# Optimization experiments

Hardware: AMD Instinct MI355X
Metric: run time of the kernel (lower is better)

## Reference

```python
import jax, jax.numpy as jnp
import numpy as np

B, S, D, H = 512, 128, 2, 512


def _lstm_cell(x, h, c, Wih, Whh, bih, bhh):
    # PyTorch gate order: i, f, g, o
    z = x @ Wih.T + h @ Whh.T + bih + bhh
    i, f, g, o = jnp.split(z, 4, axis=-1)
    c = jax.nn.sigmoid(f) * c + jax.nn.sigmoid(i) * jnp.tanh(g)
    h = jax.nn.sigmoid(o) * jnp.tanh(c)
    return h, c


def setup_inputs() -> dict:
    key = jax.random.key(0)
    ks = jax.random.split(key, 18)
    sc = 1.0 / np.sqrt(H)
    u = lambda k, shape: jax.random.uniform(k, shape, jnp.float32, -sc, sc)
    return {
        "inp": jax.random.normal(ks[0], (B, S, D), jnp.float32),
        "enc_Wih": u(ks[1], (4 * H, D)),
        "enc_Whh": u(ks[2], (4 * H, H)),
        "enc_bih": u(ks[3], (4 * H,)),
        "enc_bhh": u(ks[4], (4 * H,)),
        "dec_Wih": u(ks[5], (4 * H, D)),
        "dec_Whh": u(ks[6], (4 * H, H)),
        "dec_bih": u(ks[7], (4 * H,)),
        "dec_bhh": u(ks[8], (4 * H,)),
        "W1": u(ks[9], (H, H)),
        "b1": u(ks[10], (H,)),
        "W2": u(ks[11], (H, H)),
        "b2": u(ks[12], (H,)),
        "v_w": u(ks[13], (H,)),
        "v_b": u(ks[14], (1,)),
        "comb_W": u(ks[15], (H, 2 * H)),
        "comb_b": u(ks[16], (H,)),
    }


def reference(inp, enc_Wih, enc_Whh, enc_bih, enc_bhh,
              dec_Wih, dec_Whh, dec_bih, dec_bhh,
              W1, b1, W2, b2, v_w, v_b, comb_W, comb_b):
    Bb, Ss, _ = inp.shape
    xs = jnp.transpose(inp, (1, 0, 2))  # [S,B,D]

    # --- encoder LSTM (1 layer) ---
    def enc_step(carry, x):
        h, c = carry
        h, c = _lstm_cell(x, h, c, enc_Wih, enc_Whh, enc_bih, enc_bhh)
        return (h, c), h

    h0 = jnp.zeros((Bb, H), inp.dtype)
    (h_enc, c_enc), enc_out = jax.lax.scan(enc_step, (h0, h0), xs)  # enc_out: [S,B,H]

    W1e = enc_out @ W1.T + b1            # [S,B,H]
    enc_bt = jnp.transpose(enc_out, (1, 0, 2))  # [B,S,H]

    # --- pointer decoder ---
    def dec_step(carry, _):
        h, c, cur = carry
        h, c = _lstm_cell(cur, h, c, dec_Wih, dec_Whh, dec_bih, dec_bhh)
        q = h @ W2.T + b2                               # [B,H]
        u = jnp.tanh(W1e + q[None]) @ v_w + v_b[0]      # [S,B]
        a = jax.nn.softmax(u.T, axis=1)                 # [B,S]
        chosen = jnp.argmax(a, axis=1)                  # [B]
        cur = jnp.take_along_axis(inp, chosen[:, None, None], axis=1)[:, 0, :]  # [B,D]
        ctx = jnp.einsum('bs,bsh->bh', a, enc_bt)       # [B,H]
        h = jnp.concatenate([ctx, h], axis=1) @ comb_W.T + comb_b
        return (h, c, cur), a

    cur0 = jnp.full((Bb, D), -1.0, inp.dtype)
    _, outs = jax.lax.scan(dec_step, (h_enc, c_enc, cur0), None, length=Ss)
    return jnp.transpose(outs, (1, 0, 2))  # [B,S,S]
```

## Files before the change

### kernel.cpp

```cpp
#include <hip/hip_runtime.h>

#define PB 512
#define PS 128
#define PD 2
#define PH 512
#define P4H 2048

typedef unsigned int u32;
typedef unsigned short u16;
typedef __attribute__((ext_vector_type(8))) short short8;
typedef __attribute__((ext_vector_type(4))) float f32x4;

__device__ __forceinline__ float fast_sigmoid(float x) {
    return __fdividef(1.0f, 1.0f + __expf(-x));
}
__device__ __forceinline__ float fast_tanh(float x) {
    float ax = fabsf(x);
    float e = __expf(-2.0f * ax);
    float r = __fdividef(1.0f - e, 1.0f + e);
    return x < 0.0f ? -r : r;
}

__device__ __forceinline__ float bf_dec_u(u16 v) { return __uint_as_float((u32)v << 16); }
__device__ __forceinline__ u16 bf_trunc(float v) { return (u16)(__float_as_uint(v) >> 16); }
__device__ __forceinline__ u16 bf_rne(float v) {
    u32 u = __float_as_uint(v);
    return (u16)((u + 0x7FFFu + ((u >> 16) & 1u)) >> 16);
}
__device__ __forceinline__ void bf_split(float v, u16& hi, u16& lo) {
    hi = bf_trunc(v);
    lo = bf_rne(v - bf_dec_u(hi));
}

struct CF32 {
    using T = float;
    static __device__ __forceinline__ float dec(T v) { return v; }
    static __device__ __forceinline__ T enc(float v) { return v; }
    static __device__ __forceinline__ void dec4(const T* p, float* o) {
        float4 v = *(const float4*)p; o[0]=v.x; o[1]=v.y; o[2]=v.z; o[3]=v.w;
    }
};
struct CBF16 {
    using T = u16;
    static __device__ __forceinline__ float dec(T v) { return __uint_as_float((u32)v << 16); }
    static __device__ __forceinline__ T enc(float v) { return bf_rne(v); }
    static __device__ __forceinline__ void dec4(const T* p, float* o) {
        uint2 v = *(const uint2*)p;
        o[0] = __uint_as_float(v.x << 16);
        o[1] = __uint_as_float(v.x & 0xFFFF0000u);
        o[2] = __uint_as_float(v.y << 16);
        o[3] = __uint_as_float(v.y & 0xFFFF0000u);
    }
};

__global__ __launch_bounds__(256) void prep_whh(
    const float* __restrict__ Whh, u16* __restrict__ hi, u16* __restrict__ lo)
{
    int np = blockIdx.x;
    int j = np >> 2, g = np & 3;
    const float* src = Whh + (size_t)(g * PH + j) * PH;
    for (int k = threadIdx.x; k < PH; k += 256) {
        u16 h_, l_;
        bf_split(src[k], h_, l_);
        hi[(size_t)np * PH + k] = h_;
        lo[(size_t)np * PH + k] = l_;
    }
}
__global__ __launch_bounds__(256) void prep_split(
    const float* __restrict__ W, u16* __restrict__ hi, u16* __restrict__ lo, int K)
{
    int n = blockIdx.x;
    const float* src = W + (size_t)n * K;
    for (int k = threadIdx.x; k < K; k += 256) {
        u16 h_, l_;
        bf_split(src[k], h_, l_);
        hi[(size_t)n * K + k] = h_;
        lo[(size_t)n * K + k] = l_;
    }
}
__global__ __launch_bounds__(256) void prep_small(
    const float* __restrict__ Wih, const float* __restrict__ bih,
    const float* __restrict__ bhh, float* __restrict__ wihp, float* __restrict__ bs)
{
    int np = blockIdx.x * 256 + threadIdx.x;
    if (np >= P4H) return;
    int j = np >> 2, g = np & 3;
    int n = g * PH + j;
    wihp[np * 2]     = Wih[(size_t)n * PD];
    wihp[np * 2 + 1] = Wih[(size_t)n * PD + 1];
    bs[np] = bih[n] + bhh[n];
}

template<int EXTRA_MODE>
__global__ __launch_bounds__(256) void lstm_fused(
    const u16* __restrict__ Whh_hi, const u16* __restrict__ Whh_lo,
    const float* __restrict__ wih_perm, const float* __restrict__ bsum,
    const float* __restrict__ x, int x_stride,
    const float* __restrict__ h_in,
    float* __restrict__ cT,
    float* __restrict__ h_out,
    void* __restrict__ extra)
{
    __shared__ u16 As_hi[64][72];
    __shared__ u16 As_lo[64][72];
    __shared__ u16 Bs_hi[64][72];
    __shared__ u16 Bs_lo[64][72];

    const int tid = threadIdx.x;
    const int bb = blockIdx.x * 64;
    const int bn = blockIdx.y * 64;
    const int w = tid >> 6;
    const int wm = w >> 1, wn = w & 1;
    const int lane = tid & 63;
    const int l15 = lane & 15, lq = lane >> 4;

    f32x4 acc[2][2];
    #pragma unroll
    for (int i = 0; i < 2; ++i)
        #pragma unroll
        for (int j = 0; j < 2; ++j)
            acc[i][j] = (f32x4)0.0f;

    for (int k0 = 0; k0 < PH; k0 += 64) {
        #pragma unroll
        for (int rep = 0; rep < 2; ++rep) {
            int chunk = tid + rep * 256;
            int row = chunk >> 3, kc = (chunk & 7) * 8;
            *(uint4*)&As_hi[row][kc] = *(const uint4*)&Whh_hi[(size_t)(bn + row) * PH + k0 + kc];
            *(uint4*)&As_lo[row][kc] = *(const uint4*)&Whh_lo[(size_t)(bn + row) * PH + k0 + kc];
        }
        #pragma unroll
        for (int rep = 0; rep < 4; ++rep) {
            int chunk = tid + rep * 256;
            int row = chunk >> 4, kc = (chunk & 15) * 4;
            float4 v = *(const float4*)&h_in[(size_t)(bb + row) * PH + k0 + kc];
            u16 h0_, l0_, h1_, l1_, h2_, l2_, h3_, l3_;
            bf_split(v.x, h0_, l0_); bf_split(v.y, h1_, l1_);
            bf_split(v.z, h2_, l2_); bf_split(v.w, h3_, l3_);
            *(uint2*)&Bs_hi[row][kc] = make_uint2((u32)h0_ | ((u32)h1_ << 16),
                                                  (u32)h2_ | ((u32)h3_ << 16));
            *(uint2*)&Bs_lo[row][kc] = make_uint2((u32)l0_ | ((u32)l1_ << 16),
                                                  (u32)l2_ | ((u32)l3_ << 16));
        }
        __syncthreads();
        #pragma unroll
        for (int ks = 0; ks < 2; ++ks) {
            int kk = ks * 32 + lq * 8;
            short8 ah[2], al[2], bh[2], bl[2];
            #pragma unroll
            for (int mf = 0; mf < 2; ++mf) {
                int r = wm * 32 + mf * 16 + l15;
                ah[mf] = *(const short8*)&As_hi[r][kk];
                al[mf] = *(const short8*)&As_lo[r][kk];
            }
            #pragma unroll
            for (int nf = 0; nf < 2; ++nf) {
                int r = wn * 32 + nf * 16 + l15;
                bh[nf] = *(const short8*)&Bs_hi[r][kk];
                bl[nf] = *(const short8*)&Bs_lo[r][kk];
            }
            #pragma unroll
            for (int mf = 0; mf < 2; ++mf)
                #pragma unroll
                for (int nf = 0; nf < 2; ++nf) {
                    acc[mf][nf] = __builtin_amdgcn_mfma_f32_16x16x32_bf16(ah[mf], bh[nf], acc[mf][nf], 0, 0, 0);
                    acc[mf][nf] = __builtin_amdgcn_mfma_f32_16x16x32_bf16(ah[mf], bl[nf], acc[mf][nf], 0, 0, 0);
                    acc[mf][nf] = __builtin_amdgcn_mfma_f32_16x16x32_bf16(al[mf], bh[nf], acc[mf][nf], 0, 0, 0);
                }
        }
        __syncthreads();
    }

    float* Hs = (float*)&As_hi[0][0];
    #pragma unroll
    for (int nf = 0; nf < 2; ++nf) {
        int b_loc = wn * 32 + nf * 16 + l15;
        int b = bb + b_loc;
        float x0 = x[b * x_stride];
        float x1 = x[b * x_stride + 1];
        #pragma unroll
        for (int mf = 0; mf < 2; ++mf) {
            int np_loc = wm * 32 + mf * 16 + lq * 4;
            int np = bn + np_loc;
            float4 b4 = *(const float4*)&bsum[np];
            float4 wA = *(const float4*)&wih_perm[np * 2];
            float4 wB = *(const float4*)&wih_perm[np * 2 + 4];
            float zi = acc[mf][nf][0] + b4.x + x0 * wA.x + x1 * wA.y;
            float zf = acc[mf][nf][1] + b4.y + x0 * wA.z + x1 * wA.w;
            float zg = acc[mf][nf][2] + b4.z + x0 * wB.x + x1 * wB.y;
            float zo = acc[mf][nf][3] + b4.w + x0 * wB.z + x1 * wB.w;
            int jg = np >> 2;
            float cold = cT[(size_t)jg * PB + b];
            float cv = fast_sigmoid(zf) * cold + fast_sigmoid(zi) * fast_tanh(zg);
            float hv = fast_sigmoid(zo) * fast_tanh(cv);
            cT[(size_t)jg * PB + b] = cv;
            Hs[(np_loc >> 2) * 66 + b_loc] = hv;
        }
    }
    __syncthreads();
    {
        int b_loc = tid >> 2, jp = (tid & 3) * 4;
        int b = bb + b_loc;
        int jbase = bn >> 2;
        float4 hv4;
        hv4.x = Hs[(jp + 0) * 66 + b_loc];
        hv4.y = Hs[(jp + 1) * 66 + b_loc];
        hv4.z = Hs[(jp + 2) * 66 + b_loc];
        hv4.w = Hs[(jp + 3) * 66 + b_loc];
        *(float4*)&h_out[(size_t)b * PH + jbase + jp] = hv4;
        if (EXTRA_MODE == 1) {
            u16* e = (u16*)extra;
            *(uint2*)&e[(size_t)b * PH + jbase + jp] =
                make_uint2((u32)bf_rne(hv4.x) | ((u32)bf_rne(hv4.y) << 16),
                           (u32)bf_rne(hv4.z) | ((u32)bf_rne(hv4.w) << 16));
        } else if (EXTRA_MODE == 2) {
            float* e = (float*)extra;
            *(float4*)&e[(size_t)b * (2 * PH) + PH + jbase + jp] = hv4;
        }
    }
}

template<int ACT_F32, int OUT_BF16>
__global__ __launch_bounds__(256) void gemm_wtA(
    const u16* __restrict__ Whi, const u16* __restrict__ Wlo,
    const void* __restrict__ act, const float* __restrict__ bias,
    void* __restrict__ out, int K, int ldo)
{
    __shared__ u16 As_hi[64][72];
    __shared__ u16 As_lo[64][72];
    __shared__ u16 Bs_hi[64][72];
    __shared__ u16 Bs_lo[64][72];

    const int tid = threadIdx.x;
    const int bm = blockIdx.x * 64;
    const int bn = blockIdx.y * 64;
    const int w = tid >> 6;
    const int wm = w >> 1, wn = w & 1;
    const int lane = tid & 63;
    const int l15 = lane & 15, lq = lane >> 4;

    f32x4 acc[2][2];
    #pragma unroll
    for (int i = 0; i < 2; ++i)
        #pragma unroll
        for (int j = 0; j < 2; ++j)
            acc[i][j] = (f32x4)0.0f;

    for (int k0 = 0; k0 < K; k0 += 64) {
        #pragma unroll
        for (int rep = 0; rep < 2; ++rep) {
            int chunk = tid + rep * 256;
            int row = chunk >> 3, kc = (chunk & 7) * 8;
            *(uint4*)&As_hi[row][kc] = *(const uint4*)&Whi[(size_t)(bn + row) * K + k0 + kc];
            *(uint4*)&As_lo[row][kc] = *(const uint4*)&Wlo[(size_t)(bn + row) * K + k0 + kc];
        }
        if (ACT_F32) {
            const float* a = (const float*)act;
            #pragma unroll
            for (int rep = 0; rep < 4; ++rep) {
                int chunk = tid + rep * 256;
                int row = chunk >> 4, kc = (chunk & 15) * 4;
                float4 v = *(const float4*)&a[(size_t)(bm + row) * K + k0 + kc];
                u16 h0_, l0_, h1_, l1_, h2_, l2_, h3_, l3_;
                bf_split(v.x, h0_, l0_); bf_split(v.y, h1_, l1_);
                bf_split(v.z, h2_, l2_); bf_split(v.w, h3_, l3_);
                *(uint2*)&Bs_hi[row][kc] = make_uint2((u32)h0_ | ((u32)h1_ << 16),
                                                      (u32)h2_ | ((u32)h3_ << 16));
                *(uint2*)&Bs_lo[row][kc] = make_uint2((u32)l0_ | ((u32)l1_ << 16),
                                                      (u32)l2_ | ((u32)l3_ << 16));
            }
        } else {
            const u16* a = (const u16*)act;
            #pragma unroll
            for (int rep = 0; rep < 2; ++rep) {
                int chunk = tid + rep * 256;
                int row = chunk >> 3, kc = (chunk & 7) * 8;
                *(uint4*)&Bs_hi[row][kc] = *(const uint4*)&a[(size_t)(bm + row) * K + k0 + kc];
            }
        }
        __syncthreads();
        #pragma unroll
        for (int ks = 0; ks < 2; ++ks) {
            int kk = ks * 32 + lq * 8;
            short8 ah[2], al[2], bh[2], bl[2];
            #pragma unroll
            for (int mf = 0; mf < 2; ++mf) {
                int r = wm * 32 + mf * 16 + l15;
                ah[mf] = *(const short8*)&As_hi[r][kk];
                al[mf] = *(const short8*)&As_lo[r][kk];
            }
            #pragma unroll
            for (int nf = 0; nf < 2; ++nf) {
                int r = wn * 32 + nf * 16 + l15;
                bh[nf] = *(const short8*)&Bs_hi[r][kk];
                if (ACT_F32) bl[nf] = *(const short8*)&Bs_lo[r][kk];
            }
            #pragma unroll
            for (int mf = 0; mf < 2; ++mf)
                #pragma unroll
                for (int nf = 0; nf < 2; ++nf) {
                    acc[mf][nf] = __builtin_amdgcn_mfma_f32_16x16x32_bf16(ah[mf], bh[nf], acc[mf][nf], 0, 0, 0);
                    if (ACT_F32) {
                        acc[mf][nf] = __builtin_amdgcn_mfma_f32_16x16x32_bf16(ah[mf], bl[nf], acc[mf][nf], 0, 0, 0);
                        acc[mf][nf] = __builtin_amdgcn_mfma_f32_16x16x32_bf16(al[mf], bh[nf], acc[mf][nf], 0, 0, 0);
                    } else {
                        acc[mf][nf] = __builtin_amdgcn_mfma_f32_16x16x32_bf16(al[mf], bh[nf], acc[mf][nf], 0, 0, 0);
                    }
                }
        }
        __syncthreads();
    }

    #pragma unroll
    for (int nf = 0; nf < 2; ++nf) {
        int m = bm + wn * 32 + nf * 16 + l15;
        #pragma unroll
        for (int mf = 0; mf < 2; ++mf) {
            int n = bn + wm * 32 + mf * 16 + lq * 4;
            float4 b4 = bias ? *(const float4*)&bias[n] : make_float4(0.f, 0.f, 0.f, 0.f);
            float v0 = acc[mf][nf][0] + b4.x;
            float v1 = acc[mf][nf][1] + b4.y;
            float v2 = acc[mf][nf][2] + b4.z;
            float v3 = acc[mf][nf][3] + b4.w;
            if (OUT_BF16) {
                u16* o = (u16*)out;
                *(uint2*)&o[(size_t)m * ldo + n] =
                    make_uint2((u32)bf_rne(v0) | ((u32)bf_rne(v1) << 16),
                               (u32)bf_rne(v2) | ((u32)bf_rne(v3) << 16));
            } else {
                float* o = (float*)out;
                *(float4*)&o[(size_t)m * ldo + n] = make_float4(v0, v1, v2, v3);
            }
        }
    }
}

template<class C>
__global__ __launch_bounds__(256) void u_pass(
    const typename C::T* __restrict__ W1e, const float* __restrict__ q,
    const float* __restrict__ v_w, const float* __restrict__ v_b,
    float* __restrict__ u_t)
{
    int row = blockIdx.x * 4 + (threadIdx.x >> 6);
    int lane = threadIdx.x & 63;
    int s = row >> 9;
    int b = row & (PB - 1);
    const typename C::T* wr = W1e + (size_t)row * PH + lane * 8;
    const float* qr = q + (size_t)b * PH + lane * 8;
    const float* vr = v_w + lane * 8;
    float w8[8], q8[8], v8[8];
    C::dec4(wr, w8); C::dec4(wr + 4, w8 + 4);
    CF32::dec4(qr, q8); CF32::dec4(qr + 4, q8 + 4);
    CF32::dec4(vr, v8); CF32::dec4(vr + 4, v8 + 4);
    float sum = 0.0f;
    #pragma unroll
    for (int i = 0; i < 8; ++i)
        sum += v8[i] * fast_tanh(w8[i] + q8[i]);
    #pragma unroll
    for (int off = 32; off; off >>= 1) sum += __shfl_xor(sum, off);
    if (lane == 0) u_t[b * PS + s] = sum + v_b[0];
}

__global__ __launch_bounds__(256) void softmax_step(
    const float* __restrict__ u_t, const float* __restrict__ inp,
    float* __restrict__ a_buf, float* __restrict__ out,
    float* __restrict__ cur, int t)
{
    int b = blockIdx.x * 4 + (threadIdx.x >> 6);
    int lane = threadIdx.x & 63;
    float2 uv = *(const float2*)&u_t[b * PS + lane * 2];
    float m = fmaxf(uv.x, uv.y);
    int mi = (uv.y > uv.x) ? (lane * 2 + 1) : (lane * 2);
    #pragma unroll
    for (int off = 32; off; off >>= 1) {
        float om = __shfl_xor(m, off);
        int oi = __shfl_xor(mi, off);
        if (om > m || (om == m && oi < mi)) { m = om; mi = oi; }
    }
    float e0 = __expf(uv.x - m);
    float e1 = __expf(uv.y - m);
    float ssum = e0 + e1;
    #pragma unroll
    for (int off = 32; off; off >>= 1) ssum += __shfl_xor(ssum, off);
    float inv = __fdividef(1.0f, ssum);
    float2 av = make_float2(e0 * inv, e1 * inv);
    *(float2*)&a_buf[b * PS + lane * 2] = av;
    *(float2*)&out[(size_t)b * PS * PS + (size_t)t * PS + lane * 2] = av;
    if (lane == 0) {
        cur[b * 2]     = inp[(size_t)b * PS * PD + mi * PD];
        cur[b * 2 + 1] = inp[(size_t)b * PS * PD + mi * PD + 1];
    }
}

template<class C>
__global__ __launch_bounds__(256) void ctx_kernel(
    const typename C::T* __restrict__ enc_out, const float* __restrict__ a_buf,
    float* __restrict__ catbuf)
{
    int b = blockIdx.x;
    int hidx = threadIdx.x;
    const float* ab = a_buf + b * PS;
    const typename C::T* e = enc_out + (size_t)b * PH;
    float acc0 = 0.0f, acc1 = 0.0f;
    #pragma unroll 4
    for (int s = 0; s < PS; ++s) {
        float a = ab[s];
        const typename C::T* es = e + (size_t)s * PB * PH;
        acc0 = fmaf(a, C::dec(es[hidx]), acc0);
        acc1 = fmaf(a, C::dec(es[hidx + 256]), acc1);
    }
    catbuf[(size_t)b * (2 * PH) + hidx] = acc0;
    catbuf[(size_t)b * (2 * PH) + hidx + 256] = acc1;
}

__global__ __launch_bounds__(256) void init_kernel(
    float* __restrict__ h, float* __restrict__ c, float* __restrict__ cur)
{
    int i = blockIdx.x * 256 + threadIdx.x;
    if (i < PB * PH) { h[i] = 0.0f; c[i] = 0.0f; }
    if (i < PB * PD) cur[i] = -1.0f;
}

template<class CA, class CO, int BM, int BN, int BK, int TM, int TN>
__global__ __launch_bounds__(256) void gemm_nt(
    const typename CA::T* __restrict__ A, const float* __restrict__ Bm,
    const float* __restrict__ bias, typename CO::T* __restrict__ C,
    int M, int N, int K)
{
    __shared__ float As[BK][BM];
    __shared__ float Bs[BK][BN];
    constexpr int TCOLS = BN / TN;
    constexpr int TROWS = BM / TM;
    static_assert(TCOLS * TROWS == 256, "thread tiling");
    const int tid = threadIdx.x;
    const int tc = tid % TCOLS;
    const int tr = tid / TCOLS;
    const int bm = blockIdx.y * BM;
    const int bn = blockIdx.x * BN;
    constexpr int AF4 = BM * BK / 4;
    constexpr int BF4 = BN * BK / 4;
    constexpr int KQ  = BK / 4;
    float acc[TM][TN];
    #pragma unroll
    for (int m = 0; m < TM; ++m)
        #pragma unroll
        for (int n = 0; n < TN; ++n) acc[m][n] = 0.0f;
    for (int k0 = 0; k0 < K; k0 += BK) {
        #pragma unroll
        for (int i = tid; i < AF4; i += 256) {
            int r = i / KQ, kq = i % KQ;
            float v4[4];
            CA::dec4(A + (size_t)(bm + r) * K + k0 + kq * 4, v4);
            As[kq*4+0][r] = v4[0]; As[kq*4+1][r] = v4[1];
            As[kq*4+2][r] = v4[2]; As[kq*4+3][r] = v4[3];
        }
        #pragma unroll
        for (int i = tid; i < BF4; i += 256) {
            int r = i / KQ, kq = i % KQ;
            const float4 v = *(const float4*)(Bm + (size_t)(bn + r) * K + k0 + kq * 4);
            Bs[kq*4+0][r] = v.x; Bs[kq*4+1][r] = v.y;
            Bs[kq*4+2][r] = v.z; Bs[kq*4+3][r] = v.w;
        }
        __syncthreads();
        #pragma unroll
        for (int k = 0; k < BK; ++k) {
            float av[TM], bv[TN];
            #pragma unroll
            for (int m = 0; m < TM; ++m) av[m] = As[k][tr * TM + m];
            #pragma unroll
            for (int n = 0; n < TN; ++n) bv[n] = Bs[k][tc * TN + n];
            #pragma unroll
            for (int m = 0; m < TM; ++m)
                #pragma unroll
                for (int n = 0; n < TN; ++n)
                    acc[m][n] = fmaf(av[m], bv[n], acc[m][n]);
        }
        __syncthreads();
    }
    #pragma unroll
    for (int m = 0; m < TM; ++m) {
        int row = bm + tr * TM + m;
        #pragma unroll
        for (int n = 0; n < TN; ++n) {
            int col = bn + tc * TN + n;
            float v = acc[m][n];
            if (bias) v += bias[col];
            C[(size_t)row * N + col] = CO::enc(v);
        }
    }
}

template<class CE>
__global__ __launch_bounds__(256) void lstm_cell(
    const float* __restrict__ z,
    const float* __restrict__ x, int x_stride,
    const float* __restrict__ Wih,
    const float* __restrict__ bih, const float* __restrict__ bhh,
    float* __restrict__ c, float* __restrict__ h,
    typename CE::T* __restrict__ extra, int extra_stride)
{
    int idx = blockIdx.x * 256 + threadIdx.x;
    int b = idx >> 9, j = idx & (PH - 1);
    float x0 = x[b * x_stride];
    float x1 = x[b * x_stride + 1];
    const float* zr = z + (size_t)b * P4H;
    float zi = zr[j]        + bih[j]        + bhh[j]        + x0 * Wih[2*j]          + x1 * Wih[2*j+1];
    float zf = zr[j + PH]   + bih[j + PH]   + bhh[j + PH]   + x0 * Wih[2*(j+PH)]     + x1 * Wih[2*(j+PH)+1];
    float zg = zr[j + 2*PH] + bih[j + 2*PH] + bhh[j + 2*PH] + x0 * Wih[2*(j+2*PH)]   + x1 * Wih[2*(j+2*PH)+1];
    float zo = zr[j + 3*PH] + bih[j + 3*PH] + bhh[j + 3*PH] + x0 * Wih[2*(j+3*PH)]   + x1 * Wih[2*(j+3*PH)+1];
    float cv = fast_sigmoid(zf) * c[idx] + fast_sigmoid(zi) * fast_tanh(zg);
    float hv = fast_sigmoid(zo) * fast_tanh(cv);
    c[idx] = cv;
    h[idx] = hv;
    if (extra) extra[(size_t)b * extra_stride + j] = CE::enc(hv);
}

struct Inputs {
    const float *inp, *enc_Wih, *enc_Whh, *enc_bih, *enc_bhh;
    const float *dec_Wih, *dec_Whh, *dec_bih, *dec_bhh;
    const float *W1, *b1, *W2, *b2, *v_w, *v_b, *comb_W, *comb_b;
};
static Inputs unpack(void* const* d_in) {
    Inputs in;
    in.inp = (const float*)d_in[0];
    in.enc_Wih = (const float*)d_in[1]; in.enc_Whh = (const float*)d_in[2];
    in.enc_bih = (const float*)d_in[3]; in.enc_bhh = (const float*)d_in[4];
    in.dec_Wih = (const float*)d_in[5]; in.dec_Whh = (const float*)d_in[6];
    in.dec_bih = (const float*)d_in[7]; in.dec_bhh = (const float*)d_in[8];
    in.W1 = (const float*)d_in[9];  in.b1 = (const float*)d_in[10];
    in.W2 = (const float*)d_in[11]; in.b2 = (const float*)d_in[12];
    in.v_w = (const float*)d_in[13]; in.v_b = (const float*)d_in[14];
    in.comb_W = (const float*)d_in[15]; in.comb_b = (const float*)d_in[16];
    return in;
}

static const size_t BIG = (size_t)PS * PB * PH;

static void run_mfma(const Inputs& in, float* out, void* d_ws, hipStream_t stream)
{
    char* p = (char*)d_ws;
    auto alloc = [&](size_t bytes) { char* q_ = p; p += bytes; return q_; };
    u16* enc_out = (u16*)alloc(BIG * 2);
    u16* W1e     = (u16*)alloc(BIG * 2);
    u16* whh_e_hi = (u16*)alloc((size_t)P4H * PH * 2);
    u16* whh_e_lo = (u16*)alloc((size_t)P4H * PH * 2);
    u16* whh_d_hi = (u16*)alloc((size_t)P4H * PH * 2);
    u16* whh_d_lo = (u16*)alloc((size_t)P4H * PH * 2);
    u16* w1h = (u16*)alloc((size_t)PH * PH * 2);
    u16* w1l = (u16*)alloc((size_t)PH * PH * 2);
    u16* w2h = (u16*)alloc((size_t)PH * PH * 2);
    u16* w2l = (u16*)alloc((size_t)PH * PH * 2);
    u16* cwh = (u16*)alloc((size_t)PH * 2 * PH * 2);
    u16* cwl = (u16*)alloc((size_t)PH * 2 * PH * 2);
    float* wih_e = (float*)alloc((size_t)P4H * 2 * 4);
    float* wih_d = (float*)alloc((size_t)P4H * 2 * 4);
    float* bsum_e = (float*)alloc((size_t)P4H * 4);
    float* bsum_d = (float*)alloc((size_t)P4H * 4);
    float* hpp0 = (float*)alloc((size_t)PB * PH * 4);
    float* hpp1 = (float*)alloc((size_t)PB * PH * 4);
    float* cT   = (float*)alloc((size_t)PB * PH * 4);
    float* h0   = (float*)alloc((size_t)PB * PH * 4);
    float* q    = (float*)alloc((size_t)PB * PH * 4);
    float* catbuf = (float*)alloc((size_t)PB * 2 * PH * 4);
    float* u_t  = (float*)alloc((size_t)PB * PS * 4);
    float* a_buf = (float*)alloc((size_t)PB * PS * 4);
    float* cur  = (float*)alloc((size_t)PB * PD * 4);
    float* hpp[2] = { hpp0, hpp1 };

    prep_whh<<<P4H, 256, 0, stream>>>(in.enc_Whh, whh_e_hi, whh_e_lo);
    prep_whh<<<P4H, 256, 0, stream>>>(in.dec_Whh, whh_d_hi, whh_d_lo);
    prep_split<<<PH, 256, 0, stream>>>(in.W1, w1h, w1l, PH);
    prep_split<<<PH, 256, 0, stream>>>(in.W2, w2h, w2l, PH);
    prep_split<<<PH, 256, 0, stream>>>(in.comb_W, cwh, cwl, 2 * PH);
    prep_small<<<P4H / 256, 256, 0, stream>>>(in.enc_Wih, in.enc_bih, in.enc_bhh, wih_e, bsum_e);
    prep_small<<<P4H / 256, 256, 0, stream>>>(in.dec_Wih, in.dec_bih, in.dec_bhh, wih_d, bsum_d);
    init_kernel<<<1024, 256, 0, stream>>>(hpp0, cT, cur);

    for (int s = 0; s < PS; ++s) {
        lstm_fused<1><<<dim3(PB / 64, P4H / 64), 256, 0, stream>>>(
            whh_e_hi, whh_e_lo, wih_e, bsum_e,
            in.inp + s * PD, PS * PD,
            hpp[s & 1], cT, hpp[(s + 1) & 1],
            enc_out + (size_t)s * PB * PH);
    }

    gemm_wtA<0, 1><<<dim3((PS * PB) / 64, PH / 64), 256, 0, stream>>>(
        w1h, w1l, enc_out, in.b1, W1e, PH, PH);

    for (int t = 0; t < PS; ++t) {
        lstm_fused<2><<<dim3(PB / 64, P4H / 64), 256, 0, stream>>>(
            whh_d_hi, whh_d_lo, wih_d, bsum_d,
            cur, PD,
            hpp[t & 1], cT, h0, catbuf);
        gemm_wtA<1, 0><<<dim3(PB / 64, PH / 64), 256, 0, stream>>>(
            w2h, w2l, h0, in.b2, q, PH, PH);
        u_pass<CBF16><<<(PS * PB) / 4, 256, 0, stream>>>(W1e, q, in.v_w, in.v_b, u_t);
        softmax_step<<<PB / 4, 256, 0, stream>>>(u_t, in.inp, a_buf, out, cur, t);
        ctx_kernel<CBF16><<<PB, 256, 0, stream>>>(enc_out, a_buf, catbuf);
        gemm_wtA<1, 0><<<dim3(PB / 64, PH / 64), 256, 0, stream>>>(
            cwh, cwl, catbuf, in.comb_b, hpp[(t + 1) & 1], 2 * PH, PH);
    }
}

static void run_fallback(const Inputs& in, float* out, void* d_ws, hipStream_t stream)
{
    char* p = (char*)d_ws;
    u16* enc_out = (u16*)p;  p += BIG * 2;
    u16* W1e     = (u16*)p;  p += BIG * 2;
    float* ws = (float*)p;
    size_t off = 0;
    auto alloc = [&](size_t n) { float* q_ = ws + off; off += n; return q_; };
    float* z      = alloc((size_t)PB * P4H);
    float* h      = alloc((size_t)PB * PH);
    float* c      = alloc((size_t)PB * PH);
    float* h0     = alloc((size_t)PB * PH);
    float* q      = alloc((size_t)PB * PH);
    float* catbuf = alloc((size_t)PB * 2 * PH);
    float* u_t    = alloc((size_t)PB * PS);
    float* a_buf  = alloc((size_t)PB * PS);
    float* cur    = alloc((size_t)PB * PD);

    init_kernel<<<1024, 256, 0, stream>>>(h, c, cur);
    for (int s = 0; s < PS; ++s) {
        gemm_nt<CF32, CF32, 64, 64, 32, 4, 4><<<dim3(P4H / 64, PB / 64), 256, 0, stream>>>(
            h, in.enc_Whh, nullptr, z, PB, P4H, PH);
        lstm_cell<CBF16><<<1024, 256, 0, stream>>>(
            z, in.inp + s * PD, PS * PD, in.enc_Wih, in.enc_bih, in.enc_bhh,
            c, h, enc_out + (size_t)s * PB * PH, PH);
    }
    gemm_nt<CBF16, CBF16, 64, 64, 32, 4, 4><<<dim3(PH / 64, (PS * PB) / 64), 256, 0, stream>>>(
        enc_out, in.W1, in.b1, W1e, PS * PB, PH, PH);
    for (int t = 0; t < PS; ++t) {
        gemm_nt<CF32, CF32, 64, 64, 32, 4, 4><<<dim3(P4H / 64, PB / 64), 256, 0, stream>>>(
            h, in.dec_Whh, nullptr, z, PB, P4H, PH);
        lstm_cell<CF32><<<1024, 256, 0, stream>>>(
            z, cur, PD, in.dec_Wih, in.dec_bih, in.dec_bhh,
            c, h0, catbuf + PH, 2 * PH);
        gemm_nt<CF32, CF32, 32, 32, 32, 2, 2><<<dim3(PH / 32, PB / 32), 256, 0, stream>>>(
            h0, in.W2, in.b2, q, PB, PH, PH);
        u_pass<CBF16><<<(PS * PB) / 4, 256, 0, stream>>>(W1e, q, in.v_w, in.v_b, u_t);
        softmax_step<<<PB / 4, 256, 0, stream>>>(u_t, in.inp, a_buf, out, cur, t);
        ctx_kernel<CBF16><<<PB, 256, 0, stream>>>(enc_out, a_buf, catbuf);
        gemm_nt<CF32, CF32, 32, 32, 32, 2, 2><<<dim3(PH / 32, PB / 32), 256, 0, stream>>>(
            catbuf, in.comb_W, in.comb_b, h, PB, PH, 2 * PH);
    }
}

extern "C" void kernel_launch(void* const* d_in, const int* in_sizes, int n_in,
                              void* d_out, int out_size, void* d_ws, size_t ws_size,
                              hipStream_t stream)
{
    Inputs in = unpack(d_in);
    float* out = (float*)d_out;

    const size_t mfma_need =
        BIG * 2 * 2 +
        (size_t)P4H * PH * 2 * 4 +
        (size_t)PH * PH * 2 * 4 +
        (size_t)PH * 2 * PH * 2 * 2 +
        (size_t)P4H * 2 * 4 * 2 +
        (size_t)P4H * 4 * 2 +
        ((size_t)PB * PH * 6 + (size_t)PB * PS * 2 + PB * PD) * 4;
    const size_t fb_need =
        BIG * 2 * 2 +
        ((size_t)PB * P4H + 4 * (size_t)PB * PH + (size_t)PB * 2 * PH +
         2 * (size_t)PB * PS + (size_t)PB * PD) * 4;

    if (ws_size >= mfma_need)      run_mfma(in, out, d_ws, stream);
    else if (ws_size >= fb_need)   run_fallback(in, out, d_ws, stream);
}
```

Measured before the change: 13.46 ms.

## Fold comb projection into decoder LSTM weights and fuse attention kernels

Precomputes a fused weight dec_Whh·comb_W (split into hi/lo bf16) and a matching fused bias, so the decoder LSTM consumes the [ctx,h] concat directly with K=1024. This removes the per-step comb_W GEMM. u_pass, softmax and ctx are merged into a single per-batch attn_fused kernel that keeps scores in shared memory, cutting launches and the u/a round trips through global memory. The encoder output layout is changed to batch-major so each attention block reads contiguous rows. Costs include a larger decoder GEMM, extra workspace, and aliasing of scratch buffers, and the reassociated matmul may alter numerics slightly.

```diff
diff --git a/kernel.cpp b/kernel.cpp
--- a/kernel.cpp
+++ b/kernel.cpp
@@ -54,16 +54,19 @@
 };
 
 __global__ __launch_bounds__(256) void prep_whh(
-    const float* __restrict__ Whh, u16* __restrict__ hi, u16* __restrict__ lo)
+    const float* __restrict__ Whh, u16* __restrict__ hi, u16* __restrict__ lo,
+    float* __restrict__ f32out)
 {
     int np = blockIdx.x;
     int j = np >> 2, g = np & 3;
     const float* src = Whh + (size_t)(g * PH + j) * PH;
     for (int k = threadIdx.x; k < PH; k += 256) {
+        float v = src[k];
         u16 h_, l_;
-        bf_split(src[k], h_, l_);
+        bf_split(v, h_, l_);
         hi[(size_t)np * PH + k] = h_;
         lo[(size_t)np * PH + k] = l_;
+        if (f32out) f32out[(size_t)np * PH + k] = v;
     }
 }
 __global__ __launch_bounds__(256) void prep_split(
@@ -78,6 +81,28 @@
         lo[(size_t)n * K + k] = l_;
     }
 }
+__global__ __launch_bounds__(256) void prep_transpose_split(
+    const float* __restrict__ W, u16* __restrict__ hi, u16* __restrict__ lo)
+{
+    __shared__ float tile[32][33];
+    int m0 = blockIdx.x * 32;
+    int k0 = blockIdx.y * 32;
+    int tx = threadIdx.x & 31, ty = threadIdx.x >> 5;
+    #pragma unroll
+    for (int i = 0; i < 4; ++i) {
+        int k = k0 + ty + i * 8;
+        tile[ty + i * 8][tx] = W[(size_t)k * (2 * PH) + m0 + tx];
+    }
+    __syncthreads();
+    #pragma unroll
+    for (int i = 0; i < 4; ++i) {
+        int m = m0 + ty + i * 8;
+        float v = tile[tx][ty + i * 8];
+        u16 h_, l_; bf_split(v, h_, l_);
+        hi[(size_t)m * PH + k0 + tx] = h_;
+        lo[(size_t)m * PH + k0 + tx] = l_;
+    }
+}
 __global__ __launch_bounds__(256) void prep_small(
     const float* __restrict__ Wih, const float* __restrict__ bih,
     const float* __restrict__ bhh, float* __restrict__ wihp, float* __restrict__ bs)
@@ -90,8 +115,23 @@
     wihp[np * 2 + 1] = Wih[(size_t)n * PD + 1];
     bs[np] = bih[n] + bhh[n];
 }
-
-template<int EXTRA_MODE>
+__global__ __launch_bounds__(256) void prep_bfused(
+    const float* __restrict__ whh_f32p, const float* __restrict__ comb_b,
+    const float* __restrict__ bsum_d, float* __restrict__ bf)
+{
+    int np = blockIdx.x * 4 + (threadIdx.x >> 6);
+    int lane = threadIdx.x & 63;
+    const float* wr = whh_f32p + (size_t)np * PH + lane * 8;
+    const float* cb = comb_b + lane * 8;
+    float s = 0.0f;
+    #pragma unroll
+    for (int i = 0; i < 8; ++i) s += wr[i] * cb[i];
+    #pragma unroll
+    for (int off = 32; off; off >>= 1) s += __shfl_xor(s, off);
+    if (lane == 0) bf[np] = s + bsum_d[np];
+}
+
+template<int EXTRA_MODE, int KK>
 __global__ __launch_bounds__(256) void lstm_fused(
     const u16* __restrict__ Whh_hi, const u16* __restrict__ Whh_lo,
     const float* __restrict__ wih_perm, const float* __restrict__ bsum,
@@ -99,7 +139,7 @@
     const float* __restrict__ h_in,
     float* __restrict__ cT,
     float* __restrict__ h_out,
-    void* __restrict__ extra)
+    void* __restrict__ extra, int ex_stride)
 {
     __shared__ u16 As_hi[64][72];
     __shared__ u16 As_lo[64][72];
@@ -121,19 +161,19 @@
         for (int j = 0; j < 2; ++j)
             acc[i][j] = (f32x4)0.0f;
 
-    for (int k0 = 0; k0 < PH; k0 += 64) {
+    for (int k0 = 0; k0 < KK; k0 += 64) {
         #pragma unroll
         for (int rep = 0; rep < 2; ++rep) {
             int chunk = tid + rep * 256;
             int row = chunk >> 3, kc = (chunk & 7) * 8;
-            *(uint4*)&As_hi[row][kc] = *(const uint4*)&Whh_hi[(size_t)(bn + row) * PH + k0 + kc];
-            *(uint4*)&As_lo[row][kc] = *(const uint4*)&Whh_lo[(size_t)(bn + row) * PH + k0 + kc];
+            *(uint4*)&As_hi[row][kc] = *(const uint4*)&Whh_hi[(size_t)(bn + row) * KK + k0 + kc];
+            *(uint4*)&As_lo[row][kc] = *(const uint4*)&Whh_lo[(size_t)(bn + row) * KK + k0 + kc];
         }
         #pragma unroll
         for (int rep = 0; rep < 4; ++rep) {
             int chunk = tid + rep * 256;
             int row = chunk >> 4, kc = (chunk & 15) * 4;
-            float4 v = *(const float4*)&h_in[(size_t)(bb + row) * PH + k0 + kc];
+            float4 v = *(const float4*)&h_in[(size_t)(bb + row) * KK + k0 + kc];
             u16 h0_, l0_, h1_, l1_, h2_, l2_, h3_, l3_;
             bf_split(v.x, h0_, l0_); bf_split(v.y, h1_, l1_);
             bf_split(v.z, h2_, l2_); bf_split(v.w, h3_, l3_);
@@ -210,21 +250,21 @@
         *(float4*)&h_out[(size_t)b * PH + jbase + jp] = hv4;
         if (EXTRA_MODE == 1) {
             u16* e = (u16*)extra;
-            *(uint2*)&e[(size_t)b * PH + jbase + jp] =
+            *(uint2*)&e[(size_t)b * ex_stride + jbase + jp] =
                 make_uint2((u32)bf_rne(hv4.x) | ((u32)bf_rne(hv4.y) << 16),
                            (u32)bf_rne(hv4.z) | ((u32)bf_rne(hv4.w) << 16));
         } else if (EXTRA_MODE == 2) {
             float* e = (float*)extra;
-            *(float4*)&e[(size_t)b * (2 * PH) + PH + jbase + jp] = hv4;
-        }
-    }
-}
-
-template<int ACT_F32, int OUT_BF16>
+            *(float4*)&e[(size_t)b * ex_stride + jbase + jp] = hv4;
+        }
+    }
+}
+
+template<int ACT_F32, int OUTMODE>
 __global__ __launch_bounds__(256) void gemm_wtA(
     const u16* __restrict__ Whi, const u16* __restrict__ Wlo,
     const void* __restrict__ act, const float* __restrict__ bias,
-    void* __restrict__ out, int K, int ldo)
+    void* __restrict__ out, void* __restrict__ out2, int K, int ldo)
 {
     __shared__ u16 As_hi[64][72];
     __shared__ u16 As_lo[64][72];
@@ -322,17 +362,103 @@
             float v1 = acc[mf][nf][1] + b4.y;
             float v2 = acc[mf][nf][2] + b4.z;
             float v3 = acc[mf][nf][3] + b4.w;
-            if (OUT_BF16) {
+            if (OUTMODE == 1) {
                 u16* o = (u16*)out;
                 *(uint2*)&o[(size_t)m * ldo + n] =
                     make_uint2((u32)bf_rne(v0) | ((u32)bf_rne(v1) << 16),
                                (u32)bf_rne(v2) | ((u32)bf_rne(v3) << 16));
+            } else if (OUTMODE == 2) {
+                u16 h0_, l0_, h1_, l1_, h2_, l2_, h3_, l3_;
+                bf_split(v0, h0_, l0_); bf_split(v1, h1_, l1_);
+                bf_split(v2, h2_, l2_); bf_split(v3, h3_, l3_);
+                u16* oh = (u16*)out;
+                u16* ol = (u16*)out2;
+                *(uint2*)&oh[(size_t)m * ldo + n] =
+                    make_uint2((u32)h0_ | ((u32)h1_ << 16), (u32)h2_ | ((u32)h3_ << 16));
+                *(uint2*)&ol[(size_t)m * ldo + n] =
+                    make_uint2((u32)l0_ | ((u32)l1_ << 16), (u32)l2_ | ((u32)l3_ << 16));
             } else {
                 float* o = (float*)out;
                 *(float4*)&o[(size_t)m * ldo + n] = make_float4(v0, v1, v2, v3);
             }
         }
     }
+}
+
+__global__ __launch_bounds__(256) void attn_fused(
+    const u16* __restrict__ W1e,
+    const u16* __restrict__ enc_out,
+    const float* __restrict__ qv,
+    const float* __restrict__ v_w, const float* __restrict__ v_b,
+    const float* __restrict__ inp,
+    float* __restrict__ out,
+    float* __restrict__ cat_out,
+    float* __restrict__ cur, int t)
+{
+    __shared__ float u_s[PS];
+    __shared__ float a_s[PS];
+    const int b = blockIdx.x;
+    const int tid = threadIdx.x;
+    const int w = tid >> 6, lane = tid & 63;
+
+    float q8[8], v8[8];
+    {
+        const float* qr = qv + (size_t)b * PH + lane * 8;
+        CF32::dec4(qr, q8); CF32::dec4(qr + 4, q8 + 4);
+        const float* vr = v_w + lane * 8;
+        CF32::dec4(vr, v8); CF32::dec4(vr + 4, v8 + 4);
+    }
+    const float vb = v_b[0];
+    const u16* wbase = W1e + (size_t)b * PS * PH + lane * 8;
+    #pragma unroll 2
+    for (int i = 0; i < 32; ++i) {
+        int s = w * 32 + i;
+        const u16* row = wbase + (size_t)s * PH;
+        float w8[8];
+        CBF16::dec4(row, w8); CBF16::dec4(row + 4, w8 + 4);
+        float sum = 0.0f;
+        #pragma unroll
+        for (int j = 0; j < 8; ++j) sum += v8[j] * fast_tanh(w8[j] + q8[j]);
+        #pragma unroll
+        for (int off = 32; off; off >>= 1) sum += __shfl_xor(sum, off);
+        if (lane == 0) u_s[s] = sum + vb;
+    }
+    __syncthreads();
+    if (w == 0) {
+        float2 uv = make_float2(u_s[lane * 2], u_s[lane * 2 + 1]);
+        float m = fmaxf(uv.x, uv.y);
+        int mi = (uv.y > uv.x) ? (lane * 2 + 1) : (lane * 2);
+        #pragma unroll
+        for (int off = 32; off; off >>= 1) {
+            float om = __shfl_xor(m, off);
+            int oi = __shfl_xor(mi, off);
+            if (om > m || (om == m && oi < mi)) { m = om; mi = oi; }
+        }
+        float e0 = __expf(uv.x - m);
+        float e1 = __expf(uv.y - m);
+        float ssum = e0 + e1;
+        #pragma unroll
+        for (int off = 32; off; off >>= 1) ssum += __shfl_xor(ssum, off);
+        float inv = __fdividef(1.0f, ssum);
+        float2 av = make_float2(e0 * inv, e1 * inv);
+        a_s[lane * 2] = av.x; a_s[lane * 2 + 1] = av.y;
+        *(float2*)&out[(size_t)b * PS * PS + (size_t)t * PS + lane * 2] = av;
+        if (lane == 0) {
+            cur[b * 2]     = inp[(size_t)b * PS * PD + mi * PD];
+            cur[b * 2 + 1] = inp[(size_t)b * PS * PD + mi * PD + 1];
+        }
+    }
+    __syncthreads();
+    float acc0 = 0.0f, acc1 = 0.0f;
+    const u16* ebase = enc_out + (size_t)b * PS * PH + tid * 2;
+    #pragma unroll 4
+    for (int s = 0; s < PS; ++s) {
+        float a = a_s[s];
+        u32 pr = *(const u32*)(ebase + (size_t)s * PH);
+        acc0 = fmaf(a, __uint_as_float(pr << 16), acc0);
+        acc1 = fmaf(a, __uint_as_float(pr & 0xFFFF0000u), acc1);
+    }
+    *(float2*)&cat_out[(size_t)b * (2 * PH) + tid * 2] = make_float2(acc0, acc1);
 }
 
 template<class C>
@@ -536,10 +662,85 @@
 
 static const size_t BIG = (size_t)PS * PB * PH;
 
+static void run_mfma2(const Inputs& in, float* out, void* d_ws, hipStream_t stream)
+{
+    char* p = (char*)d_ws;
+    auto alloc = [&](size_t bytes) { char* r = p; p += bytes; return r; };
+    u16* enc_out  = (u16*)alloc(BIG * 2);
+    u16* W1e      = (u16*)alloc(BIG * 2);
+    u16* whh_e_hi = (u16*)alloc((size_t)P4H * PH * 2);
+    u16* whh_e_lo = (u16*)alloc((size_t)P4H * PH * 2);
+    u16* whh_d_hi = (u16*)alloc((size_t)P4H * PH * 2);
+    u16* whh_d_lo = (u16*)alloc((size_t)P4H * PH * 2);
+    u16* w1h = (u16*)alloc((size_t)PH * PH * 2);
+    u16* w1l = (u16*)alloc((size_t)PH * PH * 2);
+    u16* w2h = (u16*)alloc((size_t)PH * PH * 2);
+    u16* w2l = (u16*)alloc((size_t)PH * PH * 2);
+    u16* ctw_h = (u16*)alloc((size_t)(2 * PH) * PH * 2);
+    u16* ctw_l = (u16*)alloc((size_t)(2 * PH) * PH * 2);
+    u16* wf_h = (u16*)alloc((size_t)P4H * (2 * PH) * 2);
+    u16* wf_l = (u16*)alloc((size_t)P4H * (2 * PH) * 2);
+    float* wih_e = (float*)alloc((size_t)P4H * 2 * 4);
+    float* wih_d = (float*)alloc((size_t)P4H * 2 * 4);
+    float* bsum_e = (float*)alloc((size_t)P4H * 4);
+    float* bsum_d = (float*)alloc((size_t)P4H * 4);
+    float* b_fus  = (float*)alloc((size_t)P4H * 4);
+    float* hpp0 = (float*)alloc((size_t)PB * PH * 4);
+    float* hpp1 = (float*)alloc((size_t)PB * PH * 4);
+    float* cT   = (float*)alloc((size_t)PB * PH * 4);
+    float* catreg = (float*)alloc((size_t)PB * 2 * PH * 4 * 2);
+    float* cur  = (float*)alloc((size_t)PB * PD * 4);
+    float* whh_f32p = catreg;
+    float* h0 = (float*)whh_e_hi;
+    float* q  = (float*)whh_e_lo;
+    float* cat[2] = { catreg, catreg + (size_t)PB * 2 * PH };
+    float* hpp[2] = { hpp0, hpp1 };
+
+    prep_whh<<<P4H, 256, 0, stream>>>(in.enc_Whh, whh_e_hi, whh_e_lo, nullptr);
+    prep_whh<<<P4H, 256, 0, stream>>>(in.dec_Whh, whh_d_hi, whh_d_lo, whh_f32p);
+    prep_split<<<PH, 256, 0, stream>>>(in.W1, w1h, w1l, PH);
+    prep_split<<<PH, 256, 0, stream>>>(in.W2, w2h, w2l, PH);
+    prep_transpose_split<<<dim3(32, 16), 256, 0, stream>>>(in.comb_W, ctw_h, ctw_l);
+    prep_small<<<P4H / 256, 256, 0, stream>>>(in.enc_Wih, in.enc_bih, in.enc_bhh, wih_e, bsum_e);
+    prep_small<<<P4H / 256, 256, 0, stream>>>(in.dec_Wih, in.dec_bih, in.dec_bhh, wih_d, bsum_d);
+    gemm_wtA<1, 2><<<dim3(P4H / 64, (2 * PH) / 64), 256, 0, stream>>>(
+        ctw_h, ctw_l, whh_f32p, nullptr, wf_h, wf_l, PH, 2 * PH);
+    prep_bfused<<<P4H / 4, 256, 0, stream>>>(whh_f32p, in.comb_b, bsum_d, b_fus);
+    init_kernel<<<1024, 256, 0, stream>>>(hpp0, cT, cur);
+
+    for (int s = 0; s < PS; ++s) {
+        lstm_fused<1, PH><<<dim3(PB / 64, P4H / 64), 256, 0, stream>>>(
+            whh_e_hi, whh_e_lo, wih_e, bsum_e,
+            in.inp + s * PD, PS * PD,
+            hpp[s & 1], cT, hpp[(s + 1) & 1],
+            enc_out + (size_t)s * PH, PS * PH);
+    }
+
+    gemm_wtA<0, 1><<<dim3((PS * PB) / 64, PH / 64), 256, 0, stream>>>(
+        w1h, w1l, enc_out, in.b1, W1e, nullptr, PH, PH);
+
+    for (int t = 0; t < PS; ++t) {
+        float* cat_out = cat[(t + 1) & 1];
+        if (t == 0) {
+            lstm_fused<2, PH><<<dim3(PB / 64, P4H / 64), 256, 0, stream>>>(
+                whh_d_hi, whh_d_lo, wih_d, bsum_d,
+                cur, PD, hpp[0], cT, h0, cat_out + PH, 2 * PH);
+        } else {
+            lstm_fused<2, 2 * PH><<<dim3(PB / 64, P4H / 64), 256, 0, stream>>>(
+                wf_h, wf_l, wih_d, b_fus,
+                cur, PD, cat[t & 1], cT, h0, cat_out + PH, 2 * PH);
+        }
+        gemm_wtA<1, 0><<<dim3(PB / 64, PH / 64), 256, 0, stream>>>(
+            w2h, w2l, h0, in.b2, q, nullptr, PH, PH);
+        attn_fused<<<PB, 256, 0, stream>>>(
+            W1e, enc_out, q, in.v_w, in.v_b, in.inp, out, cat_out, cur, t);
+    }
+}
+
 static void run_mfma(const Inputs& in, float* out, void* d_ws, hipStream_t stream)
 {
     char* p = (char*)d_ws;
-    auto alloc = [&](size_t bytes) { char* q_ = p; p += bytes; return q_; };
+    auto alloc = [&](size_t bytes) { char* r = p; p += bytes; return r; };
     u16* enc_out = (u16*)alloc(BIG * 2);
     u16* W1e     = (u16*)alloc(BIG * 2);
     u16* whh_e_hi = (u16*)alloc((size_t)P4H * PH * 2);
@@ -567,8 +768,8 @@
     float* cur  = (float*)alloc((size_t)PB * PD * 4);
     float* hpp[2] = { hpp0, hpp1 };
 
-    prep_whh<<<P4H, 256, 0, stream>>>(in.enc_Whh, whh_e_hi, whh_e_lo);
-    prep_whh<<<P4H, 256, 0, stream>>>(in.dec_Whh, whh_d_hi, whh_d_lo);
+    prep_whh<<<P4H, 256, 0, stream>>>(in.enc_Whh, whh_e_hi, whh_e_lo, nullptr);
+    prep_whh<<<P4H, 256, 0, stream>>>(in.dec_Whh, whh_d_hi, whh_d_lo, nullptr);
     prep_split<<<PH, 256, 0, stream>>>(in.W1, w1h, w1l, PH);
     prep_split<<<PH, 256, 0, stream>>>(in.W2, w2h, w2l, PH);
     prep_split<<<PH, 256, 0, stream>>>(in.comb_W, cwh, cwl, 2 * PH);
@@ -577,28 +778,25 @@
     init_kernel<<<1024, 256, 0, stream>>>(hpp0, cT, cur);
 
     for (int s = 0; s < PS; ++s) {
-        lstm_fused<1><<<dim3(PB / 64, P4H / 64), 256, 0, stream>>>(
+        lstm_fused<1, PH><<<dim3(PB / 64, P4H / 64), 256, 0, stream>>>(
             whh_e_hi, whh_e_lo, wih_e, bsum_e,
             in.inp + s * PD, PS * PD,
             hpp[s & 1], cT, hpp[(s + 1) & 1],
-            enc_out + (size_t)s * PB * PH);
-    }
-
+            enc_out + (size_t)s * PB * PH, PH);
+    }
     gemm_wtA<0, 1><<<dim3((PS * PB) / 64, PH / 64), 256, 0, stream>>>(
-        w1h, w1l, enc_out, in.b1, W1e, PH, PH);
-
+        w1h, w1l, enc_out, in.b1, W1e, nullptr, PH, PH);
     for (int t = 0; t < PS; ++t) {
-        lstm_fused<2><<<dim3(PB / 64, P4H / 64), 256, 0, stream>>>(
+        lstm_fused<2, PH><<<dim3(PB / 64, P4H / 64), 256, 0, stream>>>(
             whh_d_hi, whh_d_lo, wih_d, bsum_d,
-            cur, PD,
-            hpp[t & 1], cT, h0, catbuf);
+            cur, PD, hpp[t & 1], cT, h0, catbuf + PH, 2 * PH);
         gemm_wtA<1, 0><<<dim3(PB / 64, PH / 64), 256, 0, stream>>>(
-            w2h, w2l, h0, in.b2, q, PH, PH);
+            w2h, w2l, h0, in.b2, q, nullptr, PH, PH);
         u_pass<CBF16><<<(PS * PB) / 4, 256, 0, stream>>>(W1e, q, in.v_w, in.v_b, u_t);
         softmax_step<<<PB / 4, 256, 0, stream>>>(u_t, in.inp, a_buf, out, cur, t);
         ctx_kernel<CBF16><<<PB, 256, 0, stream>>>(enc_out, a_buf, catbuf);
         gemm_wtA<1, 0><<<dim3(PB / 64, PH / 64), 256, 0, stream>>>(
-            cwh, cwl, catbuf, in.comb_b, hpp[(t + 1) & 1], 2 * PH, PH);
+            cwh, cwl, catbuf, in.comb_b, hpp[(t + 1) & 1], nullptr, 2 * PH, PH);
     }
 }
 
@@ -609,7 +807,7 @@
     u16* W1e     = (u16*)p;  p += BIG * 2;
     float* ws = (float*)p;
     size_t off = 0;
-    auto alloc = [&](size_t n) { float* q_ = ws + off; off += n; return q_; };
+    auto alloc = [&](size_t n) { float* r = ws + off; off += n; return r; };
     float* z      = alloc((size_t)PB * P4H);
     float* h      = alloc((size_t)PB * PH);
     float* c      = alloc((size_t)PB * PH);
@@ -653,7 +851,18 @@
     Inputs in = unpack(d_in);
     float* out = (float*)d_out;
 
-    const size_t mfma_need =
+    const size_t t1_need =
+        BIG * 2 * 2 +
+        (size_t)P4H * PH * 2 * 4 +
+        (size_t)PH * PH * 2 * 4 +
+        (size_t)(2 * PH) * PH * 2 * 2 +
+        (size_t)P4H * (2 * PH) * 2 * 2 +
+        (size_t)P4H * 2 * 4 * 2 +
+        (size_t)P4H * 4 * 3 +
+        (size_t)PB * PH * 4 * 3 +
+        (size_t)PB * 2 * PH * 4 * 2 +
+        (size_t)PB * PD * 4;
+    const size_t t2_need =
         BIG * 2 * 2 +
         (size_t)P4H * PH * 2 * 4 +
         (size_t)PH * PH * 2 * 4 +
@@ -661,11 +870,12 @@
         (size_t)P4H * 2 * 4 * 2 +
         (size_t)P4H * 4 * 2 +
         ((size_t)PB * PH * 6 + (size_t)PB * PS * 2 + PB * PD) * 4;
-    const size_t fb_need =
+    const size_t t3_need =
         BIG * 2 * 2 +
         ((size_t)PB * P4H + 4 * (size_t)PB * PH + (size_t)PB * 2 * PH +
          2 * (size_t)PB * PS + (size_t)PB * PD) * 4;
 
-    if (ws_size >= mfma_need)      run_mfma(in, out, d_ws, stream);
-    else if (ws_size >= fb_need)   run_fallback(in, out, d_ws, stream);
-}
+    if (ws_size >= t1_need)       run_mfma2(in, out, d_ws, stream);
+    else if (ws_size >= t2_need)  run_mfma(in, out, d_ws, stream);
+    else if (ws_size >= t3_need)  run_fallback(in, out, d_ws, stream);
+}
```

New measurement: 11.78 ms. -12.5%, faster.
